# Performance work log

Measured on AMD Instinct MI355X. Metric: run time of the kernel, lower is better.

Reference implementation:

```python
import jax, jax.numpy as jnp
import numpy as np
import math


def setup_inputs() -> dict:
    key = jax.random.key(0)
    B, H, CL, QL = 16, 128, 2048, 256
    k0, k1, k2 = jax.random.split(key, 3)
    context = jax.random.normal(k0, (B, H, CL), dtype=jnp.float32)
    question = jax.random.normal(k1, (B, H, QL), dtype=jnp.float32)
    c_mask = jnp.ones((B, CL), dtype=jnp.int32)
    q_mask = jnp.ones((B, QL), dtype=jnp.int32)
    lim = math.sqrt(1.0 / H)
    w = jax.random.uniform(k2, (3 * H,), minval=-lim, maxval=lim, dtype=jnp.float32)
    return {"context": context, "question": question, "c_mask": c_mask, "q_mask": q_mask, "w": w}


def reference(context, question, c_mask, q_mask, w):
    # context: (B, H, c_len), question: (B, H, q_len), w: (3H,)
    H = context.shape[1]
    ctx = jnp.transpose(context, (0, 2, 1))   # (B, c_len, H)
    qry = jnp.transpose(question, (0, 2, 1))  # (B, q_len, H)
    wq, wc, wcq = w[:H], w[H:2 * H], w[2 * H:]
    # Trilinear similarity computed directly (no (B,c,q,3H) materialization):
    # s[b,i,j] = wq.q_j + wc.c_i + wcq.(c_i*q_j); torch layout after transpose is (B, c_len, q_len)
    s = (ctx @ wc)[:, :, None] + (qry @ wq)[:, None, :] + jnp.einsum('bch,bqh->bcq', ctx * wcq, qry)
    NEG = jnp.float32(-1e30)
    s1 = jax.nn.softmax(jnp.where(q_mask[:, None, :] > 0, s, NEG), axis=2)  # softmax over q
    s2 = jax.nn.softmax(jnp.where(c_mask[:, :, None] > 0, s, NEG), axis=1)  # softmax over c
    a = jnp.einsum('bcq,bqh->bch', s1, qry)          # context-to-query attention
    l = jnp.einsum('bcq,bkq->bck', s1, s2)           # s1 @ s2^T, (B, c_len, c_len)
    b = jnp.einsum('bck,bkh->bch', l, ctx)           # query-to-context attention
    out = jnp.concatenate([ctx, a, ctx * a, ctx * b], axis=2)  # (B, c_len, 4H)
    # drop_prob=0 -> dropout is identity
    return jnp.transpose(out, (0, 2, 1))  # (B, 4H, c_len)
```

## Files before the change

kernel.cpp:

```cpp
#include <hip/hip_runtime.h>

typedef short bf16x8 __attribute__((ext_vector_type(8)));
typedef float f32x16 __attribute__((ext_vector_type(16)));
typedef float f32x4  __attribute__((ext_vector_type(4)));
typedef unsigned int u32x4 __attribute__((ext_vector_type(4)));

constexpr int B  = 16;
constexpr int H  = 128;
constexpr int CL = 2048;
constexpr int QL = 256;
constexpr int SPLITK5 = 8;
constexpr int K5SEG = CL / SPLITK5;
constexpr float SHIFT = 8.0f;

__device__ __forceinline__ unsigned short f2bf(float x) {
  unsigned u = __float_as_uint(x);
  u += 0x7fffu + ((u >> 16) & 1u);
  return (unsigned short)(u >> 16);
}
__device__ __forceinline__ float bf2f(unsigned short u) {
  return __uint_as_float((unsigned)u << 16);
}

template<int L, bool SCALE, bool WOUT>
__device__ __forceinline__ void ktrans_body(
    const float* __restrict__ src, const float* __restrict__ wbias,
    const float* __restrict__ wscale,
    unsigned short* __restrict__ dlin, unsigned short* __restrict__ dT,
    float* __restrict__ pbias, float* __restrict__ outg0,
    int bxl, int h1, int b, int tid,
    unsigned short (*T)[72], float (*P)[64]) {
  const int c0 = bxl * 64;
  const int hh = tid >> 4;
  const int cc4 = (tid & 15) * 4;
  float4 part = make_float4(0.f, 0.f, 0.f, 0.f);
  #pragma unroll
  for (int it = 0; it < 4; ++it) {
    const int hrow = it * 16 + hh;
    const int h = h1 * 64 + hrow;
    float4 v = *(const float4*)&src[((size_t)b * H + h) * L + c0 + cc4];
    const float wb = wbias[h];
    part.x = fmaf(v.x, wb, part.x); part.y = fmaf(v.y, wb, part.y);
    part.z = fmaf(v.z, wb, part.z); part.w = fmaf(v.w, wb, part.w);
    if (WOUT) {
      f32x4 t;
      t[0] = v.x; t[1] = v.y; t[2] = v.z; t[3] = v.w;
      __builtin_nontemporal_store(
          t, (f32x4*)&outg0[((size_t)b * 4 * H + h) * (size_t)CL + c0 + cc4]);
    }
    ushort4 o;
    o.x = f2bf(v.x); o.y = f2bf(v.y); o.z = f2bf(v.z); o.w = f2bf(v.w);
    *(ushort4*)&dlin[((size_t)b * H + h) * L + c0 + cc4] = o;
    ushort4 ot;
    if (SCALE) {
      const float ws = wscale[h];
      ot.x = f2bf(v.x * ws); ot.y = f2bf(v.y * ws);
      ot.z = f2bf(v.z * ws); ot.w = f2bf(v.w * ws);
    } else {
      ot = o;
    }
    *(ushort4*)&T[hrow][cc4] = ot;
  }
  *(float4*)&P[hh][cc4] = part;
  __syncthreads();
  if (tid < 64) {
    float sum = 0.f;
    #pragma unroll
    for (int i = 0; i < 16; ++i) sum += P[i][tid];
    pbias[(size_t)h1 * B * L + (size_t)b * L + c0 + tid] = sum;
  }
  #pragma unroll
  for (int it = 0; it < 4; ++it) {
    int lin = it * 256 + tid;
    int c = lin >> 4, hc = (lin & 15) * 4;
    ushort4 o;
    o.x = T[hc + 0][c]; o.y = T[hc + 1][c];
    o.z = T[hc + 2][c]; o.w = T[hc + 3][c];
    *(ushort4*)&dT[((size_t)b * L + c0 + c) * H + h1 * 64 + hc] = o;
  }
}

__global__ __launch_bounds__(256) void ktrans_all(
    const float* __restrict__ ctx, const float* __restrict__ qry,
    const float* __restrict__ w,
    unsigned short* __restrict__ ctx_bf, unsigned short* __restrict__ ctxwT,
    unsigned short* __restrict__ qry_bf, unsigned short* __restrict__ qryT,
    float* __restrict__ pct, float* __restrict__ pqt,
    float* __restrict__ out) {
  __shared__ unsigned short T[64][72];
  __shared__ float P[16][64];
  const int h1 = blockIdx.y, b = blockIdx.z, tid = threadIdx.x;
  const int bx = blockIdx.x;
  if (bx < CL / 64) {
    ktrans_body<CL, true, true>(ctx, w + H, w + 2 * H, ctx_bf, ctxwT, pct, out,
                                bx, h1, b, tid, T, P);
  } else {
    ktrans_body<QL, false, false>(qry, w, w, qry_bf, qryT, pqt, nullptr,
                                  bx - CL / 64, h1, b, tid, T, P);
  }
}

__global__ __launch_bounds__(512) void k2_score4(
    const unsigned short* __restrict__ ctxwT, const unsigned short* __restrict__ qryT,
    const float* __restrict__ pct, const float* __restrict__ pqt,
    const int* __restrict__ cmask, const int* __restrict__ qmask,
    unsigned short* __restrict__ eu,
    float* __restrict__ rsum_g, float* __restrict__ Lpart) {
  __shared__ unsigned short t2[256 * 40];
  __shared__ float stats[32][8];
  __shared__ float cmf[32];
  const int wg = blockIdx.x;
  const int b = wg & (B - 1);
  const int cblk = wg >> 4;
  const int c0 = cblk * 32;
  const int tid = threadIdx.x;
  const int w = tid >> 6;
  const int l = tid & 63;
  const int lr = l & 31, hi = l >> 5;
  const int q0 = w * 32;
  const int c = c0 + lr;

  if (tid < 32) cmf[tid] = cmask[b * CL + c0 + tid] > 0 ? 1.f : 0.f;

  const unsigned short* ap = qryT + ((size_t)b * QL + q0 + lr) * H + hi * 8;
  const unsigned short* bp = ctxwT + ((size_t)b * CL + c) * H + hi * 8;
  f32x16 acc = {};
  #pragma unroll
  for (int k = 0; k < H; k += 16) {
    bf16x8 af = *(const bf16x8*)(ap + k);
    bf16x8 bf_ = *(const bf16x8*)(bp + k);
    acc = __builtin_amdgcn_mfma_f32_32x32x16_bf16(af, bf_, acc, 0, 0, 0);
  }

  const float ct = pct[b * CL + c] + pct[B * CL + b * CL + c];

  float rs = 0.f;
  #pragma unroll
  for (int g = 0; g < 4; ++g) {
    const int qbase = q0 + 4 * hi + 8 * g;
    float4 qa = *(const float4*)&pqt[b * QL + qbase];
    float4 qb = *(const float4*)&pqt[B * QL + b * QL + qbase];
    int4 m4 = *(const int4*)&qmask[b * QL + qbase];
    float e0 = m4.x > 0 ? __expf(acc[4 * g + 0] + ct + qa.x + qb.x - SHIFT) : 0.f;
    float e1 = m4.y > 0 ? __expf(acc[4 * g + 1] + ct + qa.y + qb.y - SHIFT) : 0.f;
    float e2 = m4.z > 0 ? __expf(acc[4 * g + 2] + ct + qa.z + qb.z - SHIFT) : 0.f;
    float e3 = m4.w > 0 ? __expf(acc[4 * g + 3] + ct + qa.w + qb.w - SHIFT) : 0.f;
    rs += e0 + e1 + e2 + e3;
    t2[(qbase + 0) * 40 + lr] = f2bf(e0);
    t2[(qbase + 1) * 40 + lr] = f2bf(e1);
    t2[(qbase + 2) * 40 + lr] = f2bf(e2);
    t2[(qbase + 3) * 40 + lr] = f2bf(e3);
  }
  rs += __shfl_xor(rs, 32);
  if (hi == 0) stats[lr][w] = rs;
  __syncthreads();

  if (tid < 32) {
    float s = 0.f;
    #pragma unroll
    for (int ww = 0; ww < 8; ++ww) s += stats[tid][ww];
    rsum_g[b * CL + c0 + tid] = s;
  }
  {
    const int q = tid >> 1, co = (tid & 1) * 16;
    bf16x8 v0 = *(const bf16x8*)&t2[q * 40 + co];
    bf16x8 v1 = *(const bf16x8*)&t2[q * 40 + co + 8];
    float cs = 0.f;
    #pragma unroll
    for (int i2 = 0; i2 < 8; ++i2) {
      cs += bf2f((unsigned short)v0[i2]) * cmf[co + i2];
      cs += bf2f((unsigned short)v1[i2]) * cmf[co + 8 + i2];
    }
    cs += __shfl_xor(cs, 1);
    unsigned short* op = eu + ((size_t)b * QL + q) * CL + c0 + co;
    *(bf16x8*)op = v0;
    *(bf16x8*)(op + 8) = v1;
    if ((tid & 1) == 0) Lpart[((size_t)b * 64 + cblk) * QL + q] = cs;
  }
}

__global__ __launch_bounds__(256, 4) void k5_tpart(
    const unsigned short* __restrict__ eu,
    const unsigned short* __restrict__ ctxbf,
    const int* __restrict__ cmask,
    unsigned short* __restrict__ tpart) {
  __shared__ unsigned int cmm[K5SEG / 2];
  const int wg = blockIdx.x;
  const int b = wg & (B - 1);
  const int seg = (wg >> 4) & (SPLITK5 - 1);
  const int q0 = (wg >> 7) * 32;
  const int tid = threadIdx.x;
  if (tid < K5SEG / 2) {
    const int cbase = b * CL + seg * K5SEG + tid * 2;
    cmm[tid] = (cmask[cbase] > 0 ? 0xFFFFu : 0u) |
               (cmask[cbase + 1] > 0 ? 0xFFFF0000u : 0u);
  }
  __syncthreads();
  const int w = tid >> 6, l = tid & 63;
  const int h0 = w * 32;
  const int lr = l & 31, lg = l >> 5;
  const unsigned short* ap = eu + ((size_t)b * QL + q0 + lr) * CL + seg * K5SEG + lg * 8;
  const unsigned short* bp = ctxbf + ((size_t)b * H + h0 + lr) * CL + seg * K5SEG + lg * 8;
  f32x16 acc = {};
  #pragma unroll
  for (int k = 0; k < K5SEG; k += 16) {
    bf16x8 af = *(const bf16x8*)(ap + k);
    bf16x8 bfr = *(const bf16x8*)(bp + k);
    u32x4 mm = *(const u32x4*)&cmm[(k >> 1) + lg * 4];
    u32x4 ai = __builtin_bit_cast(u32x4, af);
    ai &= mm;
    af = __builtin_bit_cast(bf16x8, ai);
    acc = __builtin_amdgcn_mfma_f32_32x32x16_bf16(af, bfr, acc, 0, 0, 0);
  }
  unsigned short* tp = tpart + (size_t)(seg * B + b) * QL * H;
  #pragma unroll
  for (int r = 0; r < 16; ++r) {
    int qrow = (r & 3) + 8 * (r >> 2) + 4 * lg;
    tp[(size_t)(q0 + qrow) * H + h0 + lr] = f2bf(acc[r]);
  }
}

__global__ __launch_bounds__(256) void k5b_treduce(
    const unsigned short* __restrict__ tpart, const float* __restrict__ Lpart,
    unsigned short* __restrict__ tTbf) {
  __shared__ unsigned short lds[16 * 66];
  __shared__ float csum[4][64];
  __shared__ float cinv_s[64];
  const int q0 = blockIdx.x * 64, h0 = blockIdx.y * 16, b = blockIdx.z;
  const int tid = threadIdx.x;
  {
    const int qq = tid & 63, part = tid >> 6;
    float Ls = 0.f;
    #pragma unroll
    for (int k = 0; k < 16; ++k)
      Ls += Lpart[((size_t)b * 64 + part * 16 + k) * QL + q0 + qq];
    csum[part][qq] = Ls;
  }
  __syncthreads();
  if (tid < 64)
    cinv_s[tid] = 1.0f / (csum[0][tid] + csum[1][tid] + csum[2][tid] + csum[3][tid]);
  __syncthreads();
  for (int lin = tid; lin < 64 * 16; lin += 256) {
    int q = lin >> 4, h = lin & 15;
    float v = 0.f;
    #pragma unroll
    for (int sgt = 0; sgt < SPLITK5; ++sgt)
      v += bf2f(tpart[((size_t)(sgt * B + b) * QL + q0 + q) * H + h0 + h]);
    lds[h * 66 + q] = f2bf(v * cinv_s[q]);
  }
  __syncthreads();
  for (int lin = tid; lin < 16 * 64; lin += 256) {
    int h = lin >> 6, q = lin & 63;
    tTbf[((size_t)b * H + h0 + h) * QL + q0 + q] = lds[h * 66 + q];
  }
}

__device__ __forceinline__ int qswz(int q, int c) {
  return q ^ (((c >> 3) & 7) << 3);
}

__global__ __launch_bounds__(512) void kb_out(
    const unsigned short* __restrict__ eu,
    const unsigned short* __restrict__ qrybf, const unsigned short* __restrict__ tTbf,
    const unsigned short* __restrict__ ctxbf, const float* __restrict__ rsum_g,
    float* __restrict__ out) {
  __shared__ unsigned short Ps[64 * 264];
  const int wg = blockIdx.x;
  const int b = wg & (B - 1);
  const int c0 = (wg >> 4) * 64;
  const int tid = threadIdx.x;
  const int w = tid >> 6, l = tid & 63;
  const int lr = l & 31, hi = l >> 5;
  const int h0 = (w & 3) * 32;
  const int ch = (w >> 2) * 32;
  const int c = c0 + ch + lr;

  #pragma unroll
  for (int p = 0; p < 4; ++p) {
    const int lin = p * 512 + tid;
    const int q = lin >> 3, co8 = (lin & 7) * 8;
    bf16x8 v = *(const bf16x8*)&eu[((size_t)b * QL + q) * CL + c0 + co8];
    #pragma unroll
    for (int i = 0; i < 8; ++i) {
      const int cc = co8 + i;
      Ps[cc * 264 + qswz(q, cc)] = (unsigned short)v[i];
    }
  }

  const float rinv = 1.0f / rsum_g[b * CL + c];

  unsigned short cvu[16];
  {
    const unsigned short* cvp = ctxbf + (size_t)b * H * CL + c;
    #pragma unroll
    for (int r = 0; r < 16; ++r) {
      const int h = h0 + (r & 3) + 8 * (r >> 2) + 4 * hi;
      cvu[r] = cvp[(size_t)h * CL];
    }
  }
  __syncthreads();

  const unsigned short* a1p = qrybf + ((size_t)b * H + h0 + lr) * QL + hi * 8;
  const unsigned short* a2p = tTbf + ((size_t)b * H + h0 + lr) * QL + hi * 8;
  const int crow = ch + lr;
  f32x16 accA = {}, accB = {};
  #pragma unroll
  for (int kc = 0; kc < 16; ++kc) {
    bf16x8 pb = *(const bf16x8*)&Ps[crow * 264 + qswz(kc * 16 + hi * 8, crow)];
    bf16x8 a1 = *(const bf16x8*)(a1p + kc * 16);
    bf16x8 a2 = *(const bf16x8*)(a2p + kc * 16);
    accA = __builtin_amdgcn_mfma_f32_32x32x16_bf16(a1, pb, accA, 0, 0, 0);
    accB = __builtin_amdgcn_mfma_f32_32x32x16_bf16(a2, pb, accB, 0, 0, 0);
  }
  float* ob = out + (size_t)b * 4 * H * CL;
  #pragma unroll
  for (int r = 0; r < 16; ++r) {
    const int h = h0 + (r & 3) + 8 * (r >> 2) + 4 * hi;
    const float cv = bf2f(cvu[r]);
    const float av = accA[r] * rinv;
    const float bv = accB[r] * rinv;
    __builtin_nontemporal_store(av, &ob[(size_t)(H + h) * CL + c]);
    __builtin_nontemporal_store(cv * av, &ob[(size_t)(2 * H + h) * CL + c]);
    __builtin_nontemporal_store(cv * bv, &ob[(size_t)(3 * H + h) * CL + c]);
  }
}

extern "C" void kernel_launch(void* const* d_in, const int* in_sizes, int n_in,
                              void* d_out, int out_size, void* d_ws, size_t ws_size,
                              hipStream_t stream) {
  const float* context  = (const float*)d_in[0];
  const float* question = (const float*)d_in[1];
  const int*   c_mask   = (const int*)d_in[2];
  const int*   q_mask   = (const int*)d_in[3];
  const float* w        = (const float*)d_in[4];
  float* out = (float*)d_out;

  char* ws = (char*)d_ws;
  size_t off = 0;
  auto alloc = [&](size_t bytes) -> void* {
    void* p = ws + off;
    off += (bytes + 255) & ~(size_t)255;
    return p;
  };
  unsigned short* ctx_bf = (unsigned short*)alloc((size_t)B * H * CL * 2);
  unsigned short* ctxwT  = (unsigned short*)alloc((size_t)B * CL * H * 2);
  unsigned short* qry_bf = (unsigned short*)alloc((size_t)B * H * QL * 2);
  unsigned short* qryT   = (unsigned short*)alloc((size_t)B * QL * H * 2);
  unsigned short* eu     = (unsigned short*)alloc((size_t)B * QL * CL * 2);
  unsigned short* tpart  = (unsigned short*)alloc((size_t)SPLITK5 * B * QL * H * 2);
  unsigned short* tT_bf  = (unsigned short*)alloc((size_t)B * H * QL * 2);
  float* pct   = (float*)alloc((size_t)2 * B * CL * sizeof(float));
  float* pqt   = (float*)alloc((size_t)2 * B * QL * sizeof(float));
  float* rsum_ = (float*)alloc((size_t)B * CL * sizeof(float));
  float* Lpart = (float*)alloc((size_t)B * 64 * QL * sizeof(float));

  ktrans_all<<<dim3(CL / 64 + QL / 64, H / 64, B), dim3(256), 0, stream>>>(
      context, question, w, ctx_bf, ctxwT, qry_bf, qryT, pct, pqt, out);

  k2_score4<<<dim3((CL / 32) * B), dim3(512), 0, stream>>>(
      ctxwT, qryT, pct, pqt, c_mask, q_mask, eu, rsum_, Lpart);

  k5_tpart<<<dim3((QL / 32) * SPLITK5 * B), dim3(256), 0, stream>>>(
      eu, ctx_bf, c_mask, tpart);

  k5b_treduce<<<dim3(QL / 64, H / 16, B), dim3(256), 0, stream>>>(
      tpart, Lpart, tT_bf);

  kb_out<<<dim3((CL / 64) * B), dim3(512), 0, stream>>>(
      eu, qry_bf, tT_bf, ctx_bf, rsum_, out);
}
```

Measured before the change: 85.25 us.

## Make score-kernel tile handoff wave-local and split output-kernel staging into two phases

```diff
diff --git a/kernel.cpp b/kernel.cpp
--- a/kernel.cpp
+++ b/kernel.cpp
@@ -100,7 +100,7 @@
   }
 }
 
-__global__ __launch_bounds__(512) void k2_score4(
+__global__ __launch_bounds__(512) void k2_score5(
     const unsigned short* __restrict__ ctxwT, const unsigned short* __restrict__ qryT,
     const float* __restrict__ pct, const float* __restrict__ pqt,
     const int* __restrict__ cmask, const int* __restrict__ qmask,
@@ -120,7 +120,7 @@
   const int q0 = w * 32;
   const int c = c0 + lr;
 
-  if (tid < 32) cmf[tid] = cmask[b * CL + c0 + tid] > 0 ? 1.f : 0.f;
+  if (l < 32) cmf[l] = cmask[b * CL + c0 + l] > 0 ? 1.f : 0.f;
 
   const unsigned short* ap = qryT + ((size_t)b * QL + q0 + lr) * H + hi * 8;
   const unsigned short* bp = ctxwT + ((size_t)b * CL + c) * H + hi * 8;
@@ -153,16 +153,10 @@
   }
   rs += __shfl_xor(rs, 32);
   if (hi == 0) stats[lr][w] = rs;
-  __syncthreads();
-
-  if (tid < 32) {
-    float s = 0.f;
-    #pragma unroll
-    for (int ww = 0; ww < 8; ++ww) s += stats[tid][ww];
-    rsum_g[b * CL + c0 + tid] = s;
-  }
-  {
-    const int q = tid >> 1, co = (tid & 1) * 16;
+
+  __threadfence_block();
+  {
+    const int q = q0 + (l >> 1), co = (l & 1) * 16;
     bf16x8 v0 = *(const bf16x8*)&t2[q * 40 + co];
     bf16x8 v1 = *(const bf16x8*)&t2[q * 40 + co + 8];
     float cs = 0.f;
@@ -175,7 +169,14 @@
     unsigned short* op = eu + ((size_t)b * QL + q) * CL + c0 + co;
     *(bf16x8*)op = v0;
     *(bf16x8*)(op + 8) = v1;
-    if ((tid & 1) == 0) Lpart[((size_t)b * 64 + cblk) * QL + q] = cs;
+    if ((l & 1) == 0) Lpart[((size_t)b * 64 + cblk) * QL + q] = cs;
+  }
+  __syncthreads();
+  if (tid < 32) {
+    float s = 0.f;
+    #pragma unroll
+    for (int ww = 0; ww < 8; ++ww) s += stats[tid][ww];
+    rsum_g[b * CL + c0 + tid] = s;
   }
 }
 
@@ -276,7 +277,7 @@
   const int c = c0 + ch + lr;
 
   #pragma unroll
-  for (int p = 0; p < 4; ++p) {
+  for (int p = 0; p < 2; ++p) {
     const int lin = p * 512 + tid;
     const int q = lin >> 3, co8 = (lin & 7) * 8;
     bf16x8 v = *(const bf16x8*)&eu[((size_t)b * QL + q) * CL + c0 + co8];
@@ -287,8 +288,6 @@
     }
   }
 
-  const float rinv = 1.0f / rsum_g[b * CL + c];
-
   unsigned short cvu[16];
   {
     const unsigned short* cvp = ctxbf + (size_t)b * H * CL + c;
@@ -297,6 +296,18 @@
       const int h = h0 + (r & 3) + 8 * (r >> 2) + 4 * hi;
       cvu[r] = cvp[(size_t)h * CL];
     }
+  }
+  const float rinv = 1.0f / rsum_g[b * CL + c];
+
+  bf16x8 st0, st1;
+  const int lin2 = 2 * 512 + tid, lin3 = 3 * 512 + tid;
+  {
+    const int q = lin2 >> 3, co8 = (lin2 & 7) * 8;
+    st0 = *(const bf16x8*)&eu[((size_t)b * QL + q) * CL + c0 + co8];
+  }
+  {
+    const int q = lin3 >> 3, co8 = (lin3 & 7) * 8;
+    st1 = *(const bf16x8*)&eu[((size_t)b * QL + q) * CL + c0 + co8];
   }
   __syncthreads();
 
@@ -305,13 +316,41 @@
   const int crow = ch + lr;
   f32x16 accA = {}, accB = {};
   #pragma unroll
-  for (int kc = 0; kc < 16; ++kc) {
+  for (int kc = 0; kc < 8; ++kc) {
     bf16x8 pb = *(const bf16x8*)&Ps[crow * 264 + qswz(kc * 16 + hi * 8, crow)];
     bf16x8 a1 = *(const bf16x8*)(a1p + kc * 16);
     bf16x8 a2 = *(const bf16x8*)(a2p + kc * 16);
     accA = __builtin_amdgcn_mfma_f32_32x32x16_bf16(a1, pb, accA, 0, 0, 0);
     accB = __builtin_amdgcn_mfma_f32_32x32x16_bf16(a2, pb, accB, 0, 0, 0);
   }
+
+  {
+    const int q = lin2 >> 3, co8 = (lin2 & 7) * 8;
+    #pragma unroll
+    for (int i = 0; i < 8; ++i) {
+      const int cc = co8 + i;
+      Ps[cc * 264 + qswz(q, cc)] = (unsigned short)st0[i];
+    }
+  }
+  {
+    const int q = lin3 >> 3, co8 = (lin3 & 7) * 8;
+    #pragma unroll
+    for (int i = 0; i < 8; ++i) {
+      const int cc = co8 + i;
+      Ps[cc * 264 + qswz(q, cc)] = (unsigned short)st1[i];
+    }
+  }
+  __syncthreads();
+
+  #pragma unroll
+  for (int kc = 8; kc < 16; ++kc) {
+    bf16x8 pb = *(const bf16x8*)&Ps[crow * 264 + qswz(kc * 16 + hi * 8, crow)];
+    bf16x8 a1 = *(const bf16x8*)(a1p + kc * 16);
+    bf16x8 a2 = *(const bf16x8*)(a2p + kc * 16);
+    accA = __builtin_amdgcn_mfma_f32_32x32x16_bf16(a1, pb, accA, 0, 0, 0);
+    accB = __builtin_amdgcn_mfma_f32_32x32x16_bf16(a2, pb, accB, 0, 0, 0);
+  }
+
   float* ob = out + (size_t)b * 4 * H * CL;
   #pragma unroll
   for (int r = 0; r < 16; ++r) {
@@ -357,7 +396,7 @@
   ktrans_all<<<dim3(CL / 64 + QL / 64, H / 64, B), dim3(256), 0, stream>>>(
       context, question, w, ctx_bf, ctxwT, qry_bf, qryT, pct, pqt, out);
 
-  k2_score4<<<dim3((CL / 32) * B), dim3(512), 0, stream>>>(
+  k2_score5<<<dim3((CL / 32) * B), dim3(512), 0, stream>>>(
       ctxwT, qryT, pct, pqt, c_mask, q_mask, eu, rsum_, Lpart);
 
   k5_tpart<<<dim3((QL / 32) * SPLITK5 * B), dim3(256), 0, stream>>>(
```

Result: no change. 84.37 us (-1.0%).
